# Optimization experiments

Hardware: AMD Instinct MI355X
Metric: run time of the kernel (lower is better)

Reference implementation:

```python
import jax, jax.numpy as jnp
import numpy as np

N_NODES = 100000


def setup_inputs() -> dict:
    key = jax.random.key(0)
    ks = jax.random.split(key, 6)
    F_IN, F_CH, F_OUT = 64, 64, 64
    E = 1200000
    x = jax.random.normal(ks[0], (N_NODES, F_IN), dtype=jnp.float32)
    edge_index = jax.random.randint(ks[1], (2, E), 0, N_NODES, dtype=jnp.int64)
    # MLP params (PyTorch Linear default init scale ~ 1/sqrt(fan_in))
    s1 = 1.0 / np.sqrt(2 * F_IN)
    s2 = 1.0 / np.sqrt(F_CH)
    W1 = jax.random.uniform(ks[2], (2 * F_IN, F_CH), jnp.float32, -s1, s1)
    b1 = jax.random.uniform(ks[3], (F_CH,), jnp.float32, -s1, s1)
    W2 = jax.random.uniform(ks[4], (F_CH, F_OUT), jnp.float32, -s2, s2)
    b2 = jax.random.uniform(ks[5], (F_OUT,), jnp.float32, -s2, s2)
    return {"x": x, "edge_index": edge_index, "W1": W1, "b1": b1, "W2": W2, "b2": b2}


def reference(x, edge_index, W1, b1, W2, b2):
    # PyG EdgeConv with aggr='add': out_i = sum_j MLP(concat[x_i, x_j - x_i])
    src = edge_index[0]  # j (source / neighbor)
    dst = edge_index[1]  # i (target, aggregation index)
    x_i = x[dst]                     # [E, F]
    x_j = x[src]                     # [E, F]
    msg = jnp.concatenate([x_i, x_j - x_i], axis=-1)      # [E, 2F]
    h = jax.nn.relu(msg @ W1 + b1) @ W2 + b2               # [E, F_out]
    agg = jax.ops.segment_sum(h, dst, num_segments=N_NODES)  # [N, F_out]
    return jnp.tanh(agg)
```

## Files before the change

kernel.cpp:

```cpp
#include <hip/hip_runtime.h>
#include <math.h>


#define FDIM 64
#define BN 128
#define BSH 7
#define CAPB 2048
#define MAXB 1024
#define EPB 4096
#define PRE_SMEM 52224

typedef unsigned int u32;
typedef unsigned short u16;
typedef _Float16 hf;

__device__ __forceinline__ float bf_lo(u32 u) {
    union { u32 i; float f; } c; c.i = u << 16; return c.f;
}
__device__ __forceinline__ float bf_hi(u32 u) {
    union { u32 i; float f; } c; c.i = u & 0xffff0000u; return c.f;
}
__device__ __forceinline__ u32 f2bf_rne(float f) {
    union { float f; u32 u; } c; c.f = f;
    u32 u = c.u;
    u += 0x7fffu + ((u >> 16) & 1u);
    return u >> 16;
}
__device__ __forceinline__ u32 f2h(float f) {
    union { u16 s; hf h; } c; c.h = (hf)f; return (u32)c.s;
}
__device__ __forceinline__ float h_lo(u32 u) {
    union { u16 s; hf h; } c; c.s = (u16)(u & 0xffffu); return (float)c.h;
}
__device__ __forceinline__ float h_hi(u32 u) {
    union { u16 s; hf h; } c; c.s = (u16)(u >> 16); return (float)c.h;
}

__global__ __launch_bounds__(256) void prep_k(
    const float* __restrict__ x, const float* __restrict__ W1,
    const float* __restrict__ b1, u16* __restrict__ Ah,
    u16* __restrict__ Bmh, const int* __restrict__ ei,
    u32* __restrict__ slotB, int* __restrict__ gcnt,
    int N, int E, int NB, int nPre, int nBin)
{
    __shared__ __align__(16) char smem[PRE_SMEM];
    const int idx = blockIdx.x;
    const int tid = threadIdx.x;

    if ((idx % 6) == 5) {
        const int bb = idx / 6;
        if (bb >= nBin) return;
        int* histL = (int*)smem;
        int* gbase = histL + MAXB;
        const int e0 = bb * EPB;

        for (int j = tid; j < NB; j += 256) histL[j] = 0;
        __syncthreads();

        #pragma unroll
        for (int i = 0; i < EPB / 256; ++i) {
            int e = e0 + i * 256 + tid;
            if (e < E) {
                int d = ei[E + e];
                atomicAdd(&histL[d >> BSH], 1);
            }
        }
        __syncthreads();

        for (int j = tid; j < NB; j += 256) {
            int h = histL[j];
            gbase[j] = (h > 0) ? atomicAdd(&gcnt[j], h) : 0;
            histL[j] = 0;
        }
        __syncthreads();

        #pragma unroll
        for (int i = 0; i < EPB / 256; ++i) {
            int e = e0 + i * 256 + tid;
            if (e < E) {
                int s = ei[e];
                int d = ei[E + e];
                int b = d >> BSH;
                int pos = gbase[b] + atomicAdd(&histL[b], 1);
                if (pos < CAPB)
                    slotB[(size_t)b * CAPB + pos] =
                        ((u32)(d & (BN - 1)) << 20) | (u32)s;
            }
        }
        return;
    }

    const int pb = idx - idx / 6;
    if (pb >= nPre) return;
    float (*Wc)[132] = (float(*)[132])smem;
    float (*xsT)[72] = (float(*)[72])(smem + 33792);

    const int node0 = pb * 64;

    for (int i = tid; i < 64 * 128; i += 256) {
        int k = i >> 7, c = i & 127;
        int cc = c & 63;
        float wb = W1[(64 + k) * 64 + cc];
        Wc[k][c] = (c < 64) ? (W1[k * 64 + cc] - wb) : wb;
    }
    {
        const int n = tid & 63;
        const int gn = node0 + n;
        const bool ok = gn < N;
        const int kb = tid >> 6;
        #pragma unroll
        for (int j = 0; j < 16; ++j) {
            int kk = kb + 4 * j;
            xsT[kk][n] = ok ? x[(size_t)gn * 64 + kk] : 0.f;
        }
    }
    __syncthreads();

    const int ng = tid & 15, cg = tid >> 4;
    const int n0 = ng * 4, c0 = cg * 8;

    float acc[4][8];
    #pragma unroll
    for (int ci = 0; ci < 8; ++ci) {
        float init = (c0 + ci < 64) ? b1[c0 + ci] : 0.f;
        #pragma unroll
        for (int ni = 0; ni < 4; ++ni) acc[ni][ci] = init;
    }

    #pragma unroll 4
    for (int k = 0; k < 64; ++k) {
        float4 xv = *(const float4*)&xsT[k][n0];
        float4 wa = *(const float4*)&Wc[k][c0];
        float4 wb = *(const float4*)&Wc[k][c0 + 4];
        float xs[4] = {xv.x, xv.y, xv.z, xv.w};
        float ws[8] = {wa.x, wa.y, wa.z, wa.w, wb.x, wb.y, wb.z, wb.w};
        #pragma unroll
        for (int ni = 0; ni < 4; ++ni)
            #pragma unroll
            for (int ci = 0; ci < 8; ++ci)
                acc[ni][ci] += xs[ni] * ws[ci];
    }

    #pragma unroll
    for (int ni = 0; ni < 4; ++ni) {
        int n = node0 + n0 + ni;
        if (n >= N) break;
        if (c0 < 64) {
            uint4 pk;
            pk.x = f2h(acc[ni][0]) | (f2h(acc[ni][1]) << 16);
            pk.y = f2h(acc[ni][2]) | (f2h(acc[ni][3]) << 16);
            pk.z = f2h(acc[ni][4]) | (f2h(acc[ni][5]) << 16);
            pk.w = f2h(acc[ni][6]) | (f2h(acc[ni][7]) << 16);
            *(uint4*)&Ah[(size_t)n * 64 + c0] = pk;
        } else {
            uint4 pk;
            pk.x = f2bf_rne(acc[ni][0]) | (f2bf_rne(acc[ni][1]) << 16);
            pk.y = f2bf_rne(acc[ni][2]) | (f2bf_rne(acc[ni][3]) << 16);
            pk.z = f2bf_rne(acc[ni][4]) | (f2bf_rne(acc[ni][5]) << 16);
            pk.w = f2bf_rne(acc[ni][6]) | (f2bf_rne(acc[ni][7]) << 16);
            *(uint4*)&Bmh[(size_t)n * 64 + (c0 - 64)] = pk;
        }
    }
}

__device__ __forceinline__ float4 relu4add(float4 acc, float4 a, float4 b) {
    acc.x += fmaxf(a.x + b.x, 0.f);
    acc.y += fmaxf(a.y + b.y, 0.f);
    acc.z += fmaxf(a.z + b.z, 0.f);
    acc.w += fmaxf(a.w + b.w, 0.f);
    return acc;
}
__device__ __forceinline__ float4 relu4add_m(float4 acc, float4 a, float4 b, bool m) {
    acc.x += m ? fmaxf(a.x + b.x, 0.f) : 0.f;
    acc.y += m ? fmaxf(a.y + b.y, 0.f) : 0.f;
    acc.z += m ? fmaxf(a.z + b.z, 0.f) : 0.f;
    acc.w += m ? fmaxf(a.w + b.w, 0.f) : 0.f;
    return acc;
}
__device__ __forceinline__ float4 bf4(uint2 u) {
    return make_float4(bf_lo(u.x), bf_hi(u.x), bf_lo(u.y), bf_hi(u.y));
}

__global__ __launch_bounds__(256) void fused_agg(
    const u16* __restrict__ Ah, const u16* __restrict__ Bmh,
    const u32* __restrict__ slotB, const int* __restrict__ gcnt,
    const float* __restrict__ W2, const float* __restrict__ b2,
    float* __restrict__ out, int N)
{
    __shared__ __align__(16) u32 W2h[64][34];
    __shared__ __align__(16) u32 pool[BN * 17 * 2];
    __shared__ u32 csrS[CAPB];
    __shared__ int histL[BN];
    __shared__ int rowO[BN + 1];
    __shared__ int ofs[BN];
    __shared__ float b2s[64];

    u32* eStage = pool;
    uint2* aggTb = (uint2*)pool;

    const int tid = threadIdx.x;
    const int b = blockIdx.x;
    const int node0 = b * BN;
    const int cntB = min(gcnt[b], CAPB);

    for (int i = tid; i < 1024; i += 256) {
        int k = i >> 4, c4 = (i & 15) * 4;
        float4 w = *(const float4*)&W2[k * 64 + c4];
        uint2 pk;
        pk.x = f2h(w.x) | (f2h(w.y) << 16);
        pk.y = f2h(w.z) | (f2h(w.w) << 16);
        *(uint2*)&W2h[k][c4 >> 1] = pk;
    }
    if (tid < 64) b2s[tid] = b2[tid];
    if (tid < BN) histL[tid] = 0;
    __syncthreads();

    for (int i = tid; i < cntB; i += 256) {
        u32 e = slotB[(size_t)b * CAPB + i];
        eStage[i] = e;
        atomicAdd(&histL[e >> 20], 1);
    }
    __syncthreads();

    if (tid < 64) {
        int l = tid;
        int h0 = histL[2 * l], h1 = histL[2 * l + 1];
        int s = h0 + h1, inc = s;
        #pragma unroll
        for (int off = 1; off < 64; off <<= 1) {
            int t = __shfl_up(inc, off);
            if (l >= off) inc += t;
        }
        int base = inc - s;
        rowO[2 * l] = base; rowO[2 * l + 1] = base + h0;
        ofs[2 * l] = base;  ofs[2 * l + 1] = base + h0;
        if (l == 63) rowO[BN] = inc;
    }
    __syncthreads();

    for (int i = tid; i < cntB; i += 256) {
        u32 e = eStage[i];
        int pos = atomicAdd(&ofs[e >> 20], 1);
        csrS[pos] = e & 0xFFFFFu;
    }
    __syncthreads();

    {
        const int q = tid & 15, ng = tid >> 4;
        const uint2* __restrict__ B2 = (const uint2*)Bmh;
        const uint2* __restrict__ A2 = (const uint2*)Ah;
        #pragma unroll
        for (int h = 0; h < 8; ++h) {
            int nl = ng + h * 16;
            int gn = node0 + nl;
            int start = rowO[nl];
            int d = (gn < N) ? (rowO[nl + 1] - start) : 0;
            float4 a = make_float4(0.f, 0.f, 0.f, 0.f);
            if (gn < N) {
                uint2 ua = A2[(size_t)gn * 16 + q];
                a = make_float4(h_lo(ua.x), h_hi(ua.x), h_lo(ua.y), h_hi(ua.y));
            }
            float4 acc = make_float4(0.f, 0.f, 0.f, 0.f);

            int j = 0;
            for (; j + 8 <= d; j += 8) {
                int ss[8];
                uint2 bb[8];
                #pragma unroll
                for (int t = 0; t < 8; ++t) ss[t] = csrS[start + j + t];
                #pragma unroll
                for (int t = 0; t < 8; ++t) bb[t] = B2[(size_t)ss[t] * 16 + q];
                #pragma unroll
                for (int t = 0; t < 8; ++t) acc = relu4add(acc, a, bf4(bb[t]));
            }
            if (j < d) {
                int ss[8];
                uint2 bb[8];
                #pragma unroll
                for (int t = 0; t < 8; ++t) ss[t] = csrS[start + min(j + t, d - 1)];
                #pragma unroll
                for (int t = 0; t < 8; ++t) bb[t] = B2[(size_t)ss[t] * 16 + q];
                acc = relu4add(acc, a, bf4(bb[0]));
                #pragma unroll
                for (int t = 1; t < 8; ++t)
                    acc = relu4add_m(acc, a, bf4(bb[t]), j + t < d);
            }
            uint2 pk;
            pk.x = f2h(acc.x) | (f2h(acc.y) << 16);
            pk.y = f2h(acc.z) | (f2h(acc.w) << 16);
            aggTb[nl * 17 + q] = pk;
        }
    }
    __syncthreads();

    {
        const int cg = tid & 15, g0 = tid >> 4;
        const int c0 = cg * 4;
        #pragma unroll
        for (int h = 0; h < 2; ++h) {
            int g = g0 + h * 16;
            int nb0 = g * 4;
            float o[4][4];
            #pragma unroll
            for (int ni = 0; ni < 4; ++ni) {
                float dg = (float)(rowO[nb0 + ni + 1] - rowO[nb0 + ni]);
                #pragma unroll
                for (int ci = 0; ci < 4; ++ci) o[ni][ci] = dg * b2s[c0 + ci];
            }
            #pragma unroll 2
            for (int kc = 0; kc < 16; ++kc) {
                uint2 u0 = aggTb[(nb0 + 0) * 17 + kc];
                uint2 u1 = aggTb[(nb0 + 1) * 17 + kc];
                uint2 u2 = aggTb[(nb0 + 2) * 17 + kc];
                uint2 u3 = aggTb[(nb0 + 3) * 17 + kc];
                #pragma unroll
                for (int kk = 0; kk < 4; ++kk) {
                    uint2 w2p = *(const uint2*)&W2h[kc * 4 + kk][cg * 2];
                    float wv[4] = {h_lo(w2p.x), h_hi(w2p.x), h_lo(w2p.y), h_hi(w2p.y)};
                    float a0 = (kk < 2) ? ((kk == 0) ? h_lo(u0.x) : h_hi(u0.x))
                                        : ((kk == 2) ? h_lo(u0.y) : h_hi(u0.y));
                    float a1 = (kk < 2) ? ((kk == 0) ? h_lo(u1.x) : h_hi(u1.x))
                                        : ((kk == 2) ? h_lo(u1.y) : h_hi(u1.y));
                    float a2 = (kk < 2) ? ((kk == 0) ? h_lo(u2.x) : h_hi(u2.x))
                                        : ((kk == 2) ? h_lo(u2.y) : h_hi(u2.y));
                    float a3 = (kk < 2) ? ((kk == 0) ? h_lo(u3.x) : h_hi(u3.x))
                                        : ((kk == 2) ? h_lo(u3.y) : h_hi(u3.y));
                    #pragma unroll
                    for (int ci = 0; ci < 4; ++ci) {
                        o[0][ci] += a0 * wv[ci];
                        o[1][ci] += a1 * wv[ci];
                        o[2][ci] += a2 * wv[ci];
                        o[3][ci] += a3 * wv[ci];
                    }
                }
            }
            #pragma unroll
            for (int ni = 0; ni < 4; ++ni) {
                int gn = node0 + nb0 + ni;
                if (gn < N) {
                    float4 r = make_float4(tanhf(o[ni][0]), tanhf(o[ni][1]),
                                           tanhf(o[ni][2]), tanhf(o[ni][3]));
                    ((float4*)out)[(size_t)gn * 16 + cg] = r;
                }
            }
        }
    }
}

extern "C" void kernel_launch(void* const* d_in, const int* in_sizes, int n_in,
                              void* d_out, int out_size, void* d_ws, size_t ws_size,
                              hipStream_t stream)
{
    const float* x  = (const float*)d_in[0];
    const int*   ei = (const int*)d_in[1];
    const float* W1 = (const float*)d_in[2];
    const float* b1 = (const float*)d_in[3];
    const float* W2 = (const float*)d_in[4];
    const float* b2 = (const float*)d_in[5];
    float* out = (float*)d_out;

    const int N = in_sizes[0] / FDIM;
    const int E = in_sizes[1] / 2;
    const int NB = (N + BN - 1) / BN;

    u16*   Ah    = (u16*)d_ws;
    u16*   Bmh   = Ah + (size_t)N * FDIM;
    u32*   slotB = (u32*)(Bmh + (size_t)N * FDIM);
    int*   gcnt  = (int*)(slotB + (size_t)NB * CAPB);

    hipMemsetAsync(gcnt, 0, (size_t)NB * sizeof(int), stream);

    const int nPre = (N + 63) / 64;
    const int nBin = (E + EPB - 1) / EPB;
    int T = (nPre * 6 + 4) / 5;
    while (T - T / 6 < nPre) ++T;
    if (T < 6 * nBin) T = 6 * nBin;

    prep_k<<<T, 256, 0, stream>>>(x, W1, b1, Ah, Bmh, ei, slotB, gcnt,
                                  N, E, NB, nPre, nBin);
    fused_agg<<<NB, 256, 0, stream>>>(Ah, Bmh, slotB, gcnt, W2, b2, out, N);
}
```

Measured before the change: 198.7 us.

## Shrink prep shared memory with fp16 weights and coalesce x loads

The prep kernel now stores the combined W1 tile as packed fp16 pairs instead of fp32 and uses a padded transposed x tile. This cuts shared memory per block to raise occupancy, and x is now loaded with coalesced float4 reads. The binning blocks each handle twice as many edges, and the interleave ratio of binning to precompute blocks changes from 1:5 to 1:10. In exchange, W1 is rounded to fp16 before the precompute GEMM, and each bin block does more serial work.

```diff
diff --git a/kernel.cpp b/kernel.cpp
--- a/kernel.cpp
+++ b/kernel.cpp
@@ -7,8 +7,9 @@
 #define BSH 7
 #define CAPB 2048
 #define MAXB 1024
-#define EPB 4096
-#define PRE_SMEM 52224
+#define EPB 8192
+#define XS_S 65
+#define PRE_SMEM 34048
 
 typedef unsigned int u32;
 typedef unsigned short u16;
@@ -47,8 +48,8 @@
     const int idx = blockIdx.x;
     const int tid = threadIdx.x;
 
-    if ((idx % 6) == 5) {
-        const int bb = idx / 6;
+    if ((idx % 11) == 10) {
+        const int bb = idx / 11;
         if (bb >= nBin) return;
         int* histL = (int*)smem;
         int* gbase = histL + MAXB;
@@ -90,34 +91,50 @@
         return;
     }
 
-    const int pb = idx - idx / 6;
+    const int pb = idx - idx / 11;
     if (pb >= nPre) return;
-    float (*Wc)[132] = (float(*)[132])smem;
-    float (*xsT)[72] = (float(*)[72])(smem + 33792);
+    u32 (*Wch)[64] = (u32(*)[64])smem;
+    float* xsT = (float*)(smem + 64 * 64 * 4 + 512);
 
     const int node0 = pb * 64;
 
-    for (int i = tid; i < 64 * 128; i += 256) {
-        int k = i >> 7, c = i & 127;
-        int cc = c & 63;
-        float wb = W1[(64 + k) * 64 + cc];
-        Wc[k][c] = (c < 64) ? (W1[k * 64 + cc] - wb) : wb;
+    for (int i = tid; i < 64 * 64; i += 256) {
+        int k = i >> 6, p = i & 63;
+        u32 pk;
+        if (p < 32) {
+            int c = p * 2;
+            float a0 = W1[k * 64 + c]     - W1[(64 + k) * 64 + c];
+            float a1 = W1[k * 64 + c + 1] - W1[(64 + k) * 64 + c + 1];
+            pk = f2h(a0) | (f2h(a1) << 16);
+        } else {
+            int c = (p - 32) * 2;
+            float v0 = W1[(64 + k) * 64 + c];
+            float v1 = W1[(64 + k) * 64 + c + 1];
+            pk = f2h(v0) | (f2h(v1) << 16);
+        }
+        Wch[k][p] = pk;
     }
     {
-        const int n = tid & 63;
-        const int gn = node0 + n;
-        const bool ok = gn < N;
-        const int kb = tid >> 6;
-        #pragma unroll
-        for (int j = 0; j < 16; ++j) {
-            int kk = kb + 4 * j;
-            xsT[kk][n] = ok ? x[(size_t)gn * 64 + kk] : 0.f;
+        const float4* X4 = (const float4*)x;
+        #pragma unroll
+        for (int it = 0; it < 4; ++it) {
+            int i = it * 256 + tid;
+            int n = i >> 4, k4 = i & 15;
+            int gn = node0 + n;
+            float4 v = make_float4(0.f, 0.f, 0.f, 0.f);
+            if (gn < N) v = X4[(size_t)gn * 16 + k4];
+            int kb = k4 * 4;
+            xsT[(kb + 0) * XS_S + n] = v.x;
+            xsT[(kb + 1) * XS_S + n] = v.y;
+            xsT[(kb + 2) * XS_S + n] = v.z;
+            xsT[(kb + 3) * XS_S + n] = v.w;
         }
     }
     __syncthreads();
 
     const int ng = tid & 15, cg = tid >> 4;
     const int n0 = ng * 4, c0 = cg * 8;
+    const int wbase = (cg & 7) * 4 + ((cg >> 3) * 32);
 
     float acc[4][8];
     #pragma unroll
@@ -129,11 +146,13 @@
 
     #pragma unroll 4
     for (int k = 0; k < 64; ++k) {
-        float4 xv = *(const float4*)&xsT[k][n0];
-        float4 wa = *(const float4*)&Wc[k][c0];
-        float4 wb = *(const float4*)&Wc[k][c0 + 4];
-        float xs[4] = {xv.x, xv.y, xv.z, xv.w};
-        float ws[8] = {wa.x, wa.y, wa.z, wa.w, wb.x, wb.y, wb.z, wb.w};
+        float xs[4];
+        #pragma unroll
+        for (int j = 0; j < 4; ++j) xs[j] = xsT[k * XS_S + n0 + j];
+        uint2 w01 = *(const uint2*)&Wch[k][wbase];
+        uint2 w23 = *(const uint2*)&Wch[k][wbase + 2];
+        float ws[8] = {h_lo(w01.x), h_hi(w01.x), h_lo(w01.y), h_hi(w01.y),
+                       h_lo(w23.x), h_hi(w23.x), h_lo(w23.y), h_hi(w23.y)};
         #pragma unroll
         for (int ni = 0; ni < 4; ++ni)
             #pragma unroll
@@ -372,9 +391,9 @@
 
     const int nPre = (N + 63) / 64;
     const int nBin = (E + EPB - 1) / EPB;
-    int T = (nPre * 6 + 4) / 5;
-    while (T - T / 6 < nPre) ++T;
-    if (T < 6 * nBin) T = 6 * nBin;
+    int T = (nPre * 11 + 9) / 10;
+    while (T - T / 11 < nPre) ++T;
+    if (T / 11 < nBin) T = 11 * nBin;
 
     prep_k<<<T, 256, 0, stream>>>(x, W1, b1, Ah, Bmh, ei, slotB, gcnt,
                                   N, E, NB, nPre, nBin);
```

Measured after the change: 203.9 us. +2.6%, slower.
